# Kernel optimization log

Measured on AMD Instinct MI355X. Metric: run time of the kernel, lower is better.

## Reference

```python
import jax, jax.numpy as jnp
import numpy as np


def _gaussian_kernel(ksize: int, sigma: float) -> jnp.ndarray:
    # Normalized 2-D Gaussian, matching get_gaussian_kernel(ksize, sigma).
    r = jnp.arange(ksize, dtype=jnp.float32) - (ksize - 1) / 2.0
    g = jnp.exp(-(r ** 2) / (2.0 * sigma ** 2))
    k2 = jnp.outer(g, g)
    return k2 / jnp.sum(k2)


def setup_inputs() -> dict:
    key = jax.random.key(0)
    x = jax.random.normal(key, (4, 1, 2048, 2048), dtype=jnp.float32)
    # Sobel filters (ImageGradientsLayer): Ix, Iy. Shape (2, 1, 3, 3) OIHW.
    sx = jnp.array([[-1., 0., 1.], [-2., 0., 2.], [-1., 0., 1.]], dtype=jnp.float32)
    sy = sx.T
    sobel_w = jnp.stack([sx, sy])[:, None]  # (2,1,3,3)
    # Depthwise Gaussian conv weight shared across 3 channels: (3,1,7,7)
    KSIZE, SIGMA = 7, 5.0
    gk = _gaussian_kernel(KSIZE, SIGMA)
    gauss_w = jnp.tile(gk[None, None], (3, 1, 1, 1))
    return {"x": x, "sobel_w": sobel_w, "gauss_w": gauss_w}


def reference(x, sobel_w, gauss_w):
    dn = ("NCHW", "OIHW", "NCHW")
    # ImageGradientsLayer: Sobel conv, padding 1 -> (N,2,H,W)
    grads = jax.lax.conv_general_dilated(x, sobel_w, (1, 1), [(1, 1), (1, 1)],
                                         dimension_numbers=dn)
    Ix, Iy = grads[:, 0], grads[:, 1]
    # ChannelProductLayer: (N,3,H,W) = [I_xx, I_yy, I_xy]
    prods = jnp.stack([Ix * Ix, Iy * Iy, Ix * Iy], axis=1)
    # SecondMomentMatrixLayer: same 7x7 Gaussian applied per channel (depthwise)
    S = jax.lax.conv_general_dilated(prods, gauss_w, (1, 1), [(3, 3), (3, 3)],
                                     dimension_numbers=dn, feature_group_count=3)
    # NMSLayer: global lower-median threshold (torch.median semantics),
    # 7x7 stride-1 maxpool (implicit -inf padding like nn.MaxPool2d),
    # equality mask, multiply back.
    med = jnp.quantile(S, 0.5, method="lower")
    xt = jnp.where(S > med, S, jnp.zeros((), S.dtype))
    y = jax.lax.reduce_window(xt, -jnp.inf, jax.lax.max,
                              (1, 1, 7, 7), (1, 1, 1, 1),
                              [(0, 0), (0, 0), (3, 3), (3, 3)])
    mask = (xt == y).astype(xt.dtype)
    return mask * xt
```

## Files before the change

kernel.cpp:

```cpp
#include <hip/hip_runtime.h>
#include <math.h>

#define HH 2048
#define WW 2048
#define NIMG 4
#define NCH 3
#define PLANES (NIMG*NCH)
#define PIX (HH*WW)
#define TOT (PLANES*PIX)
#define W4 (WW/4)
#define MED_RANK 25165823u

struct GW { float w[7]; };

#define H1C 64
#define H23C 16
__device__ unsigned g_hist1p[H1C * 256];
__device__ unsigned g_hist2p[H23C * 4096];
__device__ unsigned g_hist3p[H23C * 4096];
__device__ unsigned g_ctrl[8];
__device__ float    g_med;

__global__ void zero_state() {
    int t = blockIdx.x * 256 + threadIdx.x;
    if (t < H1C * 256) g_hist1p[t] = 0;
    g_hist2p[t] = 0;
    g_hist3p[t] = 0;
    if (t < 8) g_ctrl[t] = 0;
    if (t == 0) g_med = 0.f;
}

__global__ __launch_bounds__(256) void sobel_gauss_h(const float* __restrict__ x,
                                                     float* __restrict__ Bh, GW g) {
    int w0 = (blockIdx.x * 256 + threadIdx.x) * 4;
    int h  = blockIdx.y;
    int n  = blockIdx.z;
    const float* xp = x + (size_t)n * PIX;
    const float* p0 = xp + (size_t)(h - 1) * WW;
    const float* p1 = xp + (size_t)h * WW;
    const float* p2 = xp + (size_t)(h + 1) * WW;
    bool has0 = (h > 0), has2 = (h < HH - 1);

    float r0[12], r1[12], r2[12];
    if (w0 >= 4 && w0 <= WW - 8) {
#pragma unroll
        for (int b = 0; b < 3; b++) {
            int col = w0 - 4 + b * 4;
            float4 v0 = has0 ? *(const float4*)(p0 + col) : make_float4(0, 0, 0, 0);
            float4 v1 = *(const float4*)(p1 + col);
            float4 v2 = has2 ? *(const float4*)(p2 + col) : make_float4(0, 0, 0, 0);
            r0[b*4+0]=v0.x; r0[b*4+1]=v0.y; r0[b*4+2]=v0.z; r0[b*4+3]=v0.w;
            r1[b*4+0]=v1.x; r1[b*4+1]=v1.y; r1[b*4+2]=v1.z; r1[b*4+3]=v1.w;
            r2[b*4+0]=v2.x; r2[b*4+1]=v2.y; r2[b*4+2]=v2.z; r2[b*4+3]=v2.w;
        }
    } else {
#pragma unroll
        for (int i = 0; i < 12; i++) {
            int col = w0 - 4 + i;
            bool okc = (col >= 0 && col < WW);
            r0[i] = (okc && has0) ? p0[col] : 0.f;
            r1[i] =  okc          ? p1[col] : 0.f;
            r2[i] = (okc && has2) ? p2[col] : 0.f;
        }
    }

    float pxx[10], pyy[10], pxy[10];
#pragma unroll
    for (int c = 0; c < 10; c++) {
        int ai = c + 1;
        int cg = w0 - 3 + c;
        float Ix = (r0[ai+1] - r0[ai-1]) + 2.f*(r1[ai+1] - r1[ai-1]) + (r2[ai+1] - r2[ai-1]);
        float Iy = (r2[ai-1] - r0[ai-1]) + 2.f*(r2[ai]   - r0[ai])   + (r2[ai+1] - r0[ai+1]);
        bool ok = (cg >= 0 && cg < WW);
        pxx[c] = ok ? Ix * Ix : 0.f;
        pyy[c] = ok ? Iy * Iy : 0.f;
        pxy[c] = ok ? Ix * Iy : 0.f;
    }

    float oxx[4], oyy[4], oxy[4];
#pragma unroll
    for (int k = 0; k < 4; k++) {
        float sxx = 0.f, syy = 0.f, sxy = 0.f;
#pragma unroll
        for (int j = 0; j < 7; j++) {
            sxx += g.w[j] * pxx[k + j];
            syy += g.w[j] * pyy[k + j];
            sxy += g.w[j] * pxy[k + j];
        }
        oxx[k] = sxx; oyy[k] = syy; oxy[k] = sxy;
    }

    size_t base = (size_t)(n * NCH) * PIX + (size_t)h * WW + w0;
    *(float4*)(Bh + base)           = make_float4(oxx[0], oxx[1], oxx[2], oxx[3]);
    *(float4*)(Bh + base + PIX)     = make_float4(oyy[0], oyy[1], oyy[2], oyy[3]);
    *(float4*)(Bh + base + 2*PIX)   = make_float4(oxy[0], oxy[1], oxy[2], oxy[3]);
}

__device__ __forceinline__ unsigned f2key(float f) {
    unsigned b = __float_as_uint(f);
    return (b & 0x80000000u) ? ~b : (b | 0x80000000u);
}

#define HCOPY 8
#define HSTRIDE 257
__global__ __launch_bounds__(256) void gauss_v_hist(const float* __restrict__ Bh,
                                                    float* __restrict__ S, GW g) {
    __shared__ unsigned lh[HCOPY * HSTRIDE];
    for (int i = threadIdx.x; i < HCOPY * HSTRIDE; i += 256) lh[i] = 0;
    __syncthreads();
    unsigned* myh = lh + (threadIdx.x & (HCOPY - 1)) * HSTRIDE;

    int e = blockIdx.x * 256 + threadIdx.x;
    int col4  = e & (W4 - 1);
    int rg    = (e >> 9) & 511;
    int plane = e >> 18;
    int rbase = rg * 4;
    const float4* bp = (const float4*)Bh + (size_t)plane * (PIX / 4) + col4;
    float4*       sp = (float4*)S        + (size_t)plane * (PIX / 4) + col4;
    const float4 zero = make_float4(0, 0, 0, 0);

    float4 t[10];
#pragma unroll
    for (int j = 0; j < 10; j++) {
        int r = rbase - 3 + j;
        t[j] = (r >= 0 && r < HH) ? bp[(size_t)r * W4] : zero;
    }
#pragma unroll
    for (int k = 0; k < 4; k++) {
        float4 acc = zero;
#pragma unroll
        for (int j = 0; j < 7; j++) {
            float w = g.w[j];
            const float4& v = t[k + j];
            acc.x += w * v.x; acc.y += w * v.y;
            acc.z += w * v.z; acc.w += w * v.w;
        }
        sp[(size_t)(rbase + k) * W4] = acc;
        unsigned bk[4] = { f2key(acc.x) >> 24, f2key(acc.y) >> 24,
                           f2key(acc.z) >> 24, f2key(acc.w) >> 24 };
#pragma unroll
        for (int q = 0; q < 4; q++) {
            unsigned first = __builtin_amdgcn_readfirstlane(bk[q]);
            unsigned long long m = __ballot(bk[q] == first);
            if (m == 0xFFFFFFFFFFFFFFFFull) {
                if ((threadIdx.x & 63) == 0) atomicAdd(&lh[first], 64u);
            } else {
                atomicAdd(&myh[bk[q]], 1u);
            }
        }
    }

    __syncthreads();
    if (threadIdx.x < 256) {
        unsigned v = 0;
#pragma unroll
        for (int c = 0; c < HCOPY; c++) v += lh[c * HSTRIDE + threadIdx.x];
        if (v) atomicAdd(&g_hist1p[(blockIdx.x & (H1C - 1)) * 256 + threadIdx.x], v);
    }
}

#define SCAN_BLOCKS 2048
#define NSTR 8
#define SLAB (TOT / 4 / NSTR)
__global__ __launch_bounds__(256) void hist_mid(const float* __restrict__ S) {
    __shared__ unsigned lh[4096];
    for (int i = threadIdx.x; i < 4096; i += 256) lh[i] = 0;
    __syncthreads();
    unsigned b1 = g_ctrl[0];
    const float4* S4 = (const float4*)S;
    long long stride = (long long)SCAN_BLOCKS * 256;
    for (long long i = (long long)blockIdx.x * 256 + threadIdx.x; i < SLAB; i += stride) {
        float4 v[NSTR];
#pragma unroll
        for (int s = 0; s < NSTR; s++) v[s] = S4[i + (long long)s * SLAB];
#pragma unroll
        for (int s = 0; s < NSTR; s++) {
            unsigned k0 = f2key(v[s].x), k1 = f2key(v[s].y),
                     k2 = f2key(v[s].z), k3 = f2key(v[s].w);
            if ((k0 >> 24) == b1) atomicAdd(&lh[(k0 >> 12) & 0xFFFu], 1u);
            if ((k1 >> 24) == b1) atomicAdd(&lh[(k1 >> 12) & 0xFFFu], 1u);
            if ((k2 >> 24) == b1) atomicAdd(&lh[(k2 >> 12) & 0xFFFu], 1u);
            if ((k3 >> 24) == b1) atomicAdd(&lh[(k3 >> 12) & 0xFFFu], 1u);
        }
    }
    __syncthreads();
    unsigned cpy = (blockIdx.x & (H23C - 1)) * 4096;
    for (int i = threadIdx.x; i < 4096; i += 256) {
        unsigned v = lh[i];
        if (v) atomicAdd(&g_hist2p[cpy + i], v);
    }
}

__global__ __launch_bounds__(256) void hist_low(const float* __restrict__ S) {
    __shared__ unsigned lh[4096];
    for (int i = threadIdx.x; i < 4096; i += 256) lh[i] = 0;
    __syncthreads();
    unsigned p2 = (g_ctrl[0] << 12) | g_ctrl[1];
    const float4* S4 = (const float4*)S;
    long long stride = (long long)SCAN_BLOCKS * 256;
    for (long long i = (long long)blockIdx.x * 256 + threadIdx.x; i < SLAB; i += stride) {
        float4 v[NSTR];
#pragma unroll
        for (int s = 0; s < NSTR; s++) v[s] = S4[i + (long long)s * SLAB];
#pragma unroll
        for (int s = 0; s < NSTR; s++) {
            unsigned k0 = f2key(v[s].x), k1 = f2key(v[s].y),
                     k2 = f2key(v[s].z), k3 = f2key(v[s].w);
            if ((k0 >> 12) == p2) atomicAdd(&lh[k0 & 0xFFFu], 1u);
            if ((k1 >> 12) == p2) atomicAdd(&lh[k1 & 0xFFFu], 1u);
            if ((k2 >> 12) == p2) atomicAdd(&lh[k2 & 0xFFFu], 1u);
            if ((k3 >> 12) == p2) atomicAdd(&lh[k3 & 0xFFFu], 1u);
        }
    }
    __syncthreads();
    unsigned cpy = (blockIdx.x & (H23C - 1)) * 4096;
    for (int i = threadIdx.x; i < 4096; i += 256) {
        unsigned v = lh[i];
        if (v) atomicAdd(&g_hist3p[cpy + i], v);
    }
}

__global__ __launch_bounds__(256) void select_k(int which) {
    __shared__ unsigned cnt[4096];
    __shared__ unsigned csum[256];
    int t = threadIdx.x;
    int nbins = (which == 0) ? 256 : 4096;
    if (which == 0) {
        unsigned s = 0;
        for (int c = 0; c < H1C; c++) s += g_hist1p[c * 256 + t];
        cnt[t] = s;
    } else {
        const unsigned* hp = (which == 1) ? g_hist2p : g_hist3p;
        for (int i = t; i < 4096; i += 256) {
            unsigned s = 0;
            for (int c = 0; c < H23C; c++) s += hp[c * 4096 + i];
            cnt[i] = s;
        }
    }
    __syncthreads();
    int per = nbins >> 8;
    unsigned s = 0;
    for (int j = 0; j < per; j++) s += cnt[t * per + j];
    csum[t] = s;
    __syncthreads();
    if (t == 0) {
        unsigned r = (which == 0) ? MED_RANK : (which == 1) ? g_ctrl[3] : g_ctrl[4];
        unsigned acc = 0; int c = 0;
        for (; c < 256; c++) { if (acc + csum[c] > r) break; acc += csum[c]; }
        int b = c * per;
        for (;; b++) { if (acc + cnt[b] > r) break; acc += cnt[b]; }
        if (which == 0)      { g_ctrl[0] = (unsigned)b; g_ctrl[3] = r - acc; }
        else if (which == 1) { g_ctrl[1] = (unsigned)b; g_ctrl[4] = r - acc; }
        else {
            g_ctrl[2] = (unsigned)b;
            unsigned key = (g_ctrl[0] << 24) | (g_ctrl[1] << 12) | (unsigned)b;
            unsigned bits = (key & 0x80000000u) ? (key ^ 0x80000000u) : ~key;
            g_med = __uint_as_float(bits);
        }
    }
}

#define OX 64
#define OY 16
__global__ __launch_bounds__(256) void nms_kernel(const float* __restrict__ S,
                                                  float* __restrict__ out) {
    __shared__ float tin[22][72];
    __shared__ float hm[22][68];
    float med = g_med;
    int plane = blockIdx.z;
    int bx = blockIdx.x * OX, by = blockIdx.y * OY;
    const float* Sp = S + (size_t)plane * PIX;
    int t = threadIdx.x;

    for (int i = t; i < 22 * 18; i += 256) {
        int r = i / 18, cc = i % 18;
        int ghh = by + r - 3;
        int gc  = bx - 4 + cc * 4;
        float4 v = make_float4(-INFINITY, -INFINITY, -INFINITY, -INFINITY);
        if (ghh >= 0 && ghh < HH && gc >= 0 && gc < WW) {
            float4 s = *(const float4*)(Sp + (size_t)ghh * WW + gc);
            v.x = (s.x > med) ? s.x : 0.f;
            v.y = (s.y > med) ? s.y : 0.f;
            v.z = (s.z > med) ? s.z : 0.f;
            v.w = (s.w > med) ? s.w : 0.f;
        }
        *(float4*)&tin[r][cc * 4] = v;
    }
    __syncthreads();

    for (int i = t; i < 22 * 16; i += 256) {
        int r = i / 16, c = i % 16;
        float a0 = tin[r][4*c+1], a1 = tin[r][4*c+2], a2 = tin[r][4*c+3];
        float a3 = tin[r][4*c+4], a4 = tin[r][4*c+5], a5 = tin[r][4*c+6];
        float a6 = tin[r][4*c+7], a7 = tin[r][4*c+8], a8 = tin[r][4*c+9];
        float a9 = tin[r][4*c+10];
        float m03 = fmaxf(fmaxf(a0, a1), fmaxf(a2, a3));
        float m36 = fmaxf(fmaxf(a3, a4), fmaxf(a5, a6));
        float4 o;
        o.x = fmaxf(m03, fmaxf(fmaxf(a4, a5), a6));
        o.y = fmaxf(fmaxf(a1, a2), fmaxf(m36, a7));
        o.z = fmaxf(fmaxf(a2, a3), fmaxf(fmaxf(a4, m36), fmaxf(a7, a8)));
        o.w = fmaxf(m36, fmaxf(fmaxf(a7, a8), a9));
        *(float4*)&hm[r][4*c] = o;
    }
    __syncthreads();

    int cc = t & 15, ro = t >> 4;
    float4 m = *(const float4*)&hm[ro][4*cc];
#pragma unroll
    for (int d = 1; d < 7; d++) {
        float4 h = *(const float4*)&hm[ro + d][4*cc];
        m.x = fmaxf(m.x, h.x); m.y = fmaxf(m.y, h.y);
        m.z = fmaxf(m.z, h.z); m.w = fmaxf(m.w, h.w);
    }
    float4 c0 = *(const float4*)&tin[ro + 3][4*cc + 4];
    float4 o;
    o.x = (c0.x == m.x) ? c0.x : 0.f;
    o.y = (c0.y == m.y) ? c0.y : 0.f;
    o.z = (c0.z == m.z) ? c0.z : 0.f;
    o.w = (c0.w == m.w) ? c0.w : 0.f;
    *(float4*)(out + (size_t)plane * PIX + (size_t)(by + ro) * WW + bx + 4*cc) = o;
}

extern "C" void kernel_launch(void* const* d_in, const int* in_sizes, int n_in,
                              void* d_out, int out_size, void* d_ws, size_t ws_size,
                              hipStream_t stream) {
    const float* x = (const float*)d_in[0];
    float* O = (float*)d_out;
    float* W = (float*)d_ws;

    GW g;
    {
        double gg[7], s = 0.0;
        for (int i = 0; i < 7; i++) { double r = i - 3.0; gg[i] = exp(-r * r / 50.0); s += gg[i]; }
        for (int i = 0; i < 7; i++) g.w[i] = (float)(gg[i] / s);
    }

    zero_state<<<256, 256, 0, stream>>>();
    sobel_gauss_h<<<dim3(WW / 1024, HH, NIMG), 256, 0, stream>>>(x, O, g);
    gauss_v_hist<<<12288, 256, 0, stream>>>(O, W, g);
    select_k<<<1, 256, 0, stream>>>(0);
    hist_mid<<<SCAN_BLOCKS, 256, 0, stream>>>(W);
    select_k<<<1, 256, 0, stream>>>(1);
    hist_low<<<SCAN_BLOCKS, 256, 0, stream>>>(W);
    select_k<<<1, 256, 0, stream>>>(2);
    nms_kernel<<<dim3(WW / OX, HH / OY, PLANES), 256, 0, stream>>>(W, O);
}
```

Before: 597.0 us.

## Fuse Sobel, horizontal and vertical Gaussian and histogram into one tiled kernel

Replaces the separate horizontal Sobel/Gaussian kernel and the vertical Gaussian/histogram kernel with one kernel that tiles 32x64 output blocks. Each block loads the input halo into shared memory, computes the horizontal pass into shared memory, then the vertical pass and the top-byte histogram. This removes the full-size global intermediate write and reread. In exchange it recomputes halo rows and columns and uses around 50KB of shared memory per block, which may limit occupancy.

```diff
diff --git a/kernel.cpp b/kernel.cpp
--- a/kernel.cpp
+++ b/kernel.cpp
@@ -30,124 +30,122 @@
     if (t == 0) g_med = 0.f;
 }
 
-__global__ __launch_bounds__(256) void sobel_gauss_h(const float* __restrict__ x,
-                                                     float* __restrict__ Bh, GW g) {
-    int w0 = (blockIdx.x * 256 + threadIdx.x) * 4;
-    int h  = blockIdx.y;
-    int n  = blockIdx.z;
+__device__ __forceinline__ unsigned f2key(float f) {
+    unsigned b = __float_as_uint(f);
+    return (b & 0x80000000u) ? ~b : (b | 0x80000000u);
+}
+
+#define HCOPY 8
+#define HSTRIDE 257
+
+__device__ __forceinline__ void hist_add(unsigned* lh, unsigned* myh, unsigned bucket) {
+    unsigned first = __builtin_amdgcn_readfirstlane(bucket);
+    unsigned long long m = __ballot(bucket == first);
+    if (m == 0xFFFFFFFFFFFFFFFFull) {
+        if ((threadIdx.x & 63) == 0) atomicAdd(&lh[first], 64u);
+    } else {
+        atomicAdd(&myh[bucket], 1u);
+    }
+}
+
+#define TX 32
+#define TY 64
+__global__ __launch_bounds__(256) void sobel_gauss_full(const float* __restrict__ x,
+                                                        float* __restrict__ S, GW g) {
+    __shared__ float xs[72][40];
+    __shared__ float bh[3][70][36];
+    __shared__ unsigned lh[HCOPY * HSTRIDE];
+    for (int i = threadIdx.x; i < HCOPY * HSTRIDE; i += 256) lh[i] = 0;
+    unsigned* myh = lh + (threadIdx.x & (HCOPY - 1)) * HSTRIDE;
+
+    int bx = blockIdx.x * TX, by = blockIdx.y * TY;
+    int n = blockIdx.z;
     const float* xp = x + (size_t)n * PIX;
-    const float* p0 = xp + (size_t)(h - 1) * WW;
-    const float* p1 = xp + (size_t)h * WW;
-    const float* p2 = xp + (size_t)(h + 1) * WW;
-    bool has0 = (h > 0), has2 = (h < HH - 1);
-
-    float r0[12], r1[12], r2[12];
-    if (w0 >= 4 && w0 <= WW - 8) {
+    int t = threadIdx.x;
+
+    for (int i = t; i < 72 * 10; i += 256) {
+        int r = i / 10, cc = i % 10;
+        int gr = by - 4 + r, gc = bx - 4 + cc * 4;
+        float4 v = make_float4(0, 0, 0, 0);
+        if (gr >= 0 && gr < HH && gc >= 0 && gc < WW)
+            v = *(const float4*)(xp + (size_t)gr * WW + gc);
+        *(float4*)&xs[r][cc * 4] = v;
+    }
+    __syncthreads();
+
+    for (int i = t; i < 70 * 8; i += 256) {
+        int r = i >> 3, c = i & 7;
+        int imgrow = by - 3 + r;
+        if (imgrow < 0 || imgrow >= HH) {
+            float4 z = make_float4(0, 0, 0, 0);
+            *(float4*)&bh[0][r][4 * c] = z;
+            *(float4*)&bh[1][r][4 * c] = z;
+            *(float4*)&bh[2][r][4 * c] = z;
+            continue;
+        }
+        float r0[12], r1[12], r2[12];
 #pragma unroll
         for (int b = 0; b < 3; b++) {
-            int col = w0 - 4 + b * 4;
-            float4 v0 = has0 ? *(const float4*)(p0 + col) : make_float4(0, 0, 0, 0);
-            float4 v1 = *(const float4*)(p1 + col);
-            float4 v2 = has2 ? *(const float4*)(p2 + col) : make_float4(0, 0, 0, 0);
+            float4 v0 = *(float4*)&xs[r][4 * c + 4 * b];
+            float4 v1 = *(float4*)&xs[r + 1][4 * c + 4 * b];
+            float4 v2 = *(float4*)&xs[r + 2][4 * c + 4 * b];
             r0[b*4+0]=v0.x; r0[b*4+1]=v0.y; r0[b*4+2]=v0.z; r0[b*4+3]=v0.w;
             r1[b*4+0]=v1.x; r1[b*4+1]=v1.y; r1[b*4+2]=v1.z; r1[b*4+3]=v1.w;
             r2[b*4+0]=v2.x; r2[b*4+1]=v2.y; r2[b*4+2]=v2.z; r2[b*4+3]=v2.w;
         }
-    } else {
-#pragma unroll
-        for (int i = 0; i < 12; i++) {
-            int col = w0 - 4 + i;
-            bool okc = (col >= 0 && col < WW);
-            r0[i] = (okc && has0) ? p0[col] : 0.f;
-            r1[i] =  okc          ? p1[col] : 0.f;
-            r2[i] = (okc && has2) ? p2[col] : 0.f;
-        }
-    }
-
-    float pxx[10], pyy[10], pxy[10];
-#pragma unroll
-    for (int c = 0; c < 10; c++) {
-        int ai = c + 1;
-        int cg = w0 - 3 + c;
-        float Ix = (r0[ai+1] - r0[ai-1]) + 2.f*(r1[ai+1] - r1[ai-1]) + (r2[ai+1] - r2[ai-1]);
-        float Iy = (r2[ai-1] - r0[ai-1]) + 2.f*(r2[ai]   - r0[ai])   + (r2[ai+1] - r0[ai+1]);
-        bool ok = (cg >= 0 && cg < WW);
-        pxx[c] = ok ? Ix * Ix : 0.f;
-        pyy[c] = ok ? Iy * Iy : 0.f;
-        pxy[c] = ok ? Ix * Iy : 0.f;
-    }
-
-    float oxx[4], oyy[4], oxy[4];
-#pragma unroll
-    for (int k = 0; k < 4; k++) {
-        float sxx = 0.f, syy = 0.f, sxy = 0.f;
+        float pxx[10], pyy[10], pxy[10];
+#pragma unroll
+        for (int p = 0; p < 10; p++) {
+            int ai = p + 1;
+            int cg = bx + 4 * c - 3 + p;
+            float Ix = (r0[ai+1] - r0[ai-1]) + 2.f*(r1[ai+1] - r1[ai-1]) + (r2[ai+1] - r2[ai-1]);
+            float Iy = (r2[ai-1] - r0[ai-1]) + 2.f*(r2[ai]   - r0[ai])   + (r2[ai+1] - r0[ai+1]);
+            bool ok = (cg >= 0 && cg < WW);
+            pxx[p] = ok ? Ix * Ix : 0.f;
+            pyy[p] = ok ? Iy * Iy : 0.f;
+            pxy[p] = ok ? Ix * Iy : 0.f;
+        }
+        float4 oxx, oyy, oxy;
+        float* ox = &oxx.x; float* oy = &oyy.x; float* oz = &oxy.x;
+#pragma unroll
+        for (int k = 0; k < 4; k++) {
+            float sxx = 0.f, syy = 0.f, sxy = 0.f;
+#pragma unroll
+            for (int j = 0; j < 7; j++) {
+                sxx += g.w[j] * pxx[k + j];
+                syy += g.w[j] * pyy[k + j];
+                sxy += g.w[j] * pxy[k + j];
+            }
+            ox[k] = sxx; oy[k] = syy; oz[k] = sxy;
+        }
+        *(float4*)&bh[0][r][4 * c] = oxx;
+        *(float4*)&bh[1][r][4 * c] = oyy;
+        *(float4*)&bh[2][r][4 * c] = oxy;
+    }
+    __syncthreads();
+
+    int cg = t & 7, ro0 = (t >> 3) * 2;
+#pragma unroll
+    for (int ch = 0; ch < 3; ch++) {
+        float4 w[8];
+#pragma unroll
+        for (int j = 0; j < 8; j++) w[j] = *(float4*)&bh[ch][ro0 + j][4 * cg];
+        float4 a0 = make_float4(0, 0, 0, 0), a1 = a0;
 #pragma unroll
         for (int j = 0; j < 7; j++) {
-            sxx += g.w[j] * pxx[k + j];
-            syy += g.w[j] * pyy[k + j];
-            sxy += g.w[j] * pxy[k + j];
-        }
-        oxx[k] = sxx; oyy[k] = syy; oxy[k] = sxy;
-    }
-
-    size_t base = (size_t)(n * NCH) * PIX + (size_t)h * WW + w0;
-    *(float4*)(Bh + base)           = make_float4(oxx[0], oxx[1], oxx[2], oxx[3]);
-    *(float4*)(Bh + base + PIX)     = make_float4(oyy[0], oyy[1], oyy[2], oyy[3]);
-    *(float4*)(Bh + base + 2*PIX)   = make_float4(oxy[0], oxy[1], oxy[2], oxy[3]);
-}
-
-__device__ __forceinline__ unsigned f2key(float f) {
-    unsigned b = __float_as_uint(f);
-    return (b & 0x80000000u) ? ~b : (b | 0x80000000u);
-}
-
-#define HCOPY 8
-#define HSTRIDE 257
-__global__ __launch_bounds__(256) void gauss_v_hist(const float* __restrict__ Bh,
-                                                    float* __restrict__ S, GW g) {
-    __shared__ unsigned lh[HCOPY * HSTRIDE];
-    for (int i = threadIdx.x; i < HCOPY * HSTRIDE; i += 256) lh[i] = 0;
-    __syncthreads();
-    unsigned* myh = lh + (threadIdx.x & (HCOPY - 1)) * HSTRIDE;
-
-    int e = blockIdx.x * 256 + threadIdx.x;
-    int col4  = e & (W4 - 1);
-    int rg    = (e >> 9) & 511;
-    int plane = e >> 18;
-    int rbase = rg * 4;
-    const float4* bp = (const float4*)Bh + (size_t)plane * (PIX / 4) + col4;
-    float4*       sp = (float4*)S        + (size_t)plane * (PIX / 4) + col4;
-    const float4 zero = make_float4(0, 0, 0, 0);
-
-    float4 t[10];
-#pragma unroll
-    for (int j = 0; j < 10; j++) {
-        int r = rbase - 3 + j;
-        t[j] = (r >= 0 && r < HH) ? bp[(size_t)r * W4] : zero;
-    }
-#pragma unroll
-    for (int k = 0; k < 4; k++) {
-        float4 acc = zero;
-#pragma unroll
-        for (int j = 0; j < 7; j++) {
-            float w = g.w[j];
-            const float4& v = t[k + j];
-            acc.x += w * v.x; acc.y += w * v.y;
-            acc.z += w * v.z; acc.w += w * v.w;
-        }
-        sp[(size_t)(rbase + k) * W4] = acc;
-        unsigned bk[4] = { f2key(acc.x) >> 24, f2key(acc.y) >> 24,
-                           f2key(acc.z) >> 24, f2key(acc.w) >> 24 };
-#pragma unroll
-        for (int q = 0; q < 4; q++) {
-            unsigned first = __builtin_amdgcn_readfirstlane(bk[q]);
-            unsigned long long m = __ballot(bk[q] == first);
-            if (m == 0xFFFFFFFFFFFFFFFFull) {
-                if ((threadIdx.x & 63) == 0) atomicAdd(&lh[first], 64u);
-            } else {
-                atomicAdd(&myh[bk[q]], 1u);
-            }
-        }
+            float gw = g.w[j];
+            a0.x += gw * w[j].x;   a0.y += gw * w[j].y;
+            a0.z += gw * w[j].z;   a0.w += gw * w[j].w;
+            a1.x += gw * w[j+1].x; a1.y += gw * w[j+1].y;
+            a1.z += gw * w[j+1].z; a1.w += gw * w[j+1].w;
+        }
+        float* sp = S + (size_t)(n * NCH + ch) * PIX;
+        *(float4*)(sp + (size_t)(by + ro0)     * WW + bx + 4 * cg) = a0;
+        *(float4*)(sp + (size_t)(by + ro0 + 1) * WW + bx + 4 * cg) = a1;
+        hist_add(lh, myh, f2key(a0.x) >> 24); hist_add(lh, myh, f2key(a0.y) >> 24);
+        hist_add(lh, myh, f2key(a0.z) >> 24); hist_add(lh, myh, f2key(a0.w) >> 24);
+        hist_add(lh, myh, f2key(a1.x) >> 24); hist_add(lh, myh, f2key(a1.y) >> 24);
+        hist_add(lh, myh, f2key(a1.z) >> 24); hist_add(lh, myh, f2key(a1.w) >> 24);
     }
 
     __syncthreads();
@@ -155,7 +153,7 @@
         unsigned v = 0;
 #pragma unroll
         for (int c = 0; c < HCOPY; c++) v += lh[c * HSTRIDE + threadIdx.x];
-        if (v) atomicAdd(&g_hist1p[(blockIdx.x & (H1C - 1)) * 256 + threadIdx.x], v);
+        if (v) atomicAdd(&g_hist1p[((blockIdx.y * 64 + blockIdx.x) & (H1C - 1)) * 256 + threadIdx.x], v);
     }
 }
 
@@ -337,8 +335,7 @@
     }
 
     zero_state<<<256, 256, 0, stream>>>();
-    sobel_gauss_h<<<dim3(WW / 1024, HH, NIMG), 256, 0, stream>>>(x, O, g);
-    gauss_v_hist<<<12288, 256, 0, stream>>>(O, W, g);
+    sobel_gauss_full<<<dim3(WW / TX, HH / TY, NIMG), 256, 0, stream>>>(x, W, g);
     select_k<<<1, 256, 0, stream>>>(0);
     hist_mid<<<SCAN_BLOCKS, 256, 0, stream>>>(W);
     select_k<<<1, 256, 0, stream>>>(1);
```

After: 517.4 us. -13.3%, faster.
